# Optimization experiments

Measured on AMD Instinct MI355X. Metric: run time of the kernel, lower is better.

The kernel has to match this reference:

```python
import jax, jax.numpy as jnp
import numpy as np

N_ENT = 100000
NUM_REL = 400  # includes inverse relations
IN_DIM = 128
OUT_DIM = 128
NUM_EDGES = 800000  # first half 'in' direction, second half 'out' direction


def setup_inputs() -> dict:
    key = jax.random.key(0)
    ks = jax.random.split(key, 10)
    s = 1.0 / np.sqrt(IN_DIM)
    return {
        "x": jax.random.normal(ks[0], (N_ENT, IN_DIM), jnp.float32),
        "r": jax.random.normal(ks[1], (NUM_REL, IN_DIM), jnp.float32),
        "edge_index": jax.random.randint(ks[2], (2, NUM_EDGES), 0, N_ENT, jnp.int32),
        "edge_type": jax.random.randint(ks[3], (NUM_EDGES,), 0, NUM_REL, jnp.int32),
        "w_in": jax.random.normal(ks[4], (IN_DIM, OUT_DIM), jnp.float32) * s,
        "w_out": jax.random.normal(ks[5], (IN_DIM, OUT_DIM), jnp.float32) * s,
        "w_loop": jax.random.normal(ks[6], (IN_DIM, OUT_DIM), jnp.float32) * s,
        "w_rel": jax.random.normal(ks[7], (IN_DIM, OUT_DIM), jnp.float32) * s,
        "loop_rel": jax.random.normal(ks[8], (1, IN_DIM), jnp.float32) * s,
        "bias": jnp.zeros((OUT_DIM,), jnp.float32),
    }


def _edge_norm(row, col, n_ent, dtype):
    # symmetric normalization deg^-1/2[row] * deg^-1/2[col], deg from row (dst) degrees
    deg = jnp.zeros((n_ent,), dtype).at[row].add(1.0)
    dinv = jnp.where(deg > 0, 1.0 / jnp.sqrt(jnp.maximum(deg, 1.0)), 0.0)
    return dinv[row] * dinv[col]


def _propagate(x, r_full, row, col, etype, w, norm):
    # gather-compose-transform-scatter: composition = sub (h_j - h_r)
    h_j = x[col]                     # [E, D]
    h_r = r_full[etype]              # [E, D]
    msg = (h_j - h_r) @ w            # [E, out_dim]
    if norm is not None:
        msg = msg * norm[:, None]
    return jnp.zeros((x.shape[0], w.shape[1]), x.dtype).at[row].add(msg)


def reference(x, r, edge_index, edge_type, w_in, w_out, w_loop, w_rel, loop_rel, bias):
    n_ent = x.shape[0]
    r_full = jnp.concatenate([r, loop_rel], axis=0)   # [R+1, D], last row = loop relation
    e_half = edge_index.shape[1] // 2
    row, col = edge_index[0], edge_index[1]

    # 'in' mode (first half of edges)
    ri, ci, ti = row[:e_half], col[:e_half], edge_type[:e_half]
    out_in = _propagate(x, r_full, ri, ci, ti, w_in, _edge_norm(ri, ci, n_ent, x.dtype))
    # 'out' mode (second half of edges)
    ro, co, to = row[e_half:], col[e_half:], edge_type[e_half:]
    out_out = _propagate(x, r_full, ro, co, to, w_out, _edge_norm(ro, co, n_ent, x.dtype))
    # 'loop' mode: self edges with loop relation, no edge norm
    loop_idx = jnp.arange(n_ent, dtype=edge_index.dtype)
    loop_type = jnp.full((n_ent,), r.shape[0], dtype=edge_type.dtype)
    out_loop = _propagate(x, r_full, loop_idx, loop_idx, loop_type, w_loop, None)

    out = (out_in + out_out + out_loop) * (1.0 / 3.0) + bias
    out = jnp.tanh(out)
    r_out = r_full[:-1] @ w_rel      # linear relation transformation (drop loop rel)
    return out, r_out
```

## Files before the change

### kernel.cpp

```cpp
#include <hip/hip_runtime.h>
#include <hip/hip_bf16.h>

#define N_ENT    100000
#define NUM_REL  400
#define DIM      128
#define NUM_EDGES 800000
#define E_HALF   400000
#define N_RB     6250
#define CAP      24

using short8 = __attribute__((ext_vector_type(8))) short;
using f32x4  = __attribute__((ext_vector_type(4))) float;

__device__ __forceinline__ float bf_lo(unsigned u) { return __uint_as_float(u << 16); }
__device__ __forceinline__ float bf_hi(unsigned u) { return __uint_as_float(u & 0xffff0000u); }
__device__ __forceinline__ unsigned short f2bf(float f) {
    unsigned u = __float_as_uint(f);
    u = u + 0x7fffu + ((u >> 16) & 1u);
    return (unsigned short)(u >> 16);
}
__device__ __forceinline__ unsigned pack2bf(float a, float b) {
    return (unsigned)f2bf(a) | ((unsigned)f2bf(b) << 16);
}

#define FB_FILL 3125
#define FB_XB   (FB_FILL + 6250)
#define FB_WT   (FB_XB + 24)
#define FB_RB   (FB_WT + 25)
#define FB_CV   (FB_RB + 1)
#define FB_REL  (FB_CV + 200)
__global__ __launch_bounds__(256) void mega_kernel(const int* __restrict__ rows,
                                                   const int* __restrict__ cols,
                                                   const int* __restrict__ et,
                                                   const float* __restrict__ x,
                                                   const float* __restrict__ w_in,
                                                   const float* __restrict__ w_out,
                                                   const float* __restrict__ w_loop,
                                                   const float* __restrict__ r,
                                                   const float* __restrict__ loop_rel,
                                                   const float* __restrict__ w_rel,
                                                   int* __restrict__ cursor,
                                                   unsigned* __restrict__ recs,
                                                   uint4* __restrict__ xb4,
                                                   uint4* __restrict__ wtfrag,
                                                   uint4* __restrict__ rb16,
                                                   float* __restrict__ cvec,
                                                   float* __restrict__ r_out) {
    int b = blockIdx.x;
    int t = threadIdx.x;
    if (b < FB_FILL) {
        int e = b * 256 + t;
        if (e < NUM_EDGES) {
            int half = (e >= E_HALF) ? 1 : 0;
            int g = half * N_ENT + rows[e];
            int col = cols[e];
            int ty = et[e];
            int pos = atomicAdd(&cursor[g], 1);
            if (pos < CAP)
                recs[(size_t)g * CAP + pos] = (unsigned)col | ((unsigned)ty << 17);
        }
    } else if (b < FB_XB) {
        int i = (b - FB_FILL) * 256 + t;
        const float* p = x + (size_t)(i >> 4) * DIM + (i & 15) * 8;
        float4 f0 = *(const float4*)p;
        float4 f1 = *(const float4*)(p + 4);
        uint4 o;
        o.x = pack2bf(f0.x, f0.y);
        o.y = pack2bf(f0.z, f0.w);
        o.z = pack2bf(f1.x, f1.y);
        o.w = pack2bf(f1.z, f1.w);
        xb4[i] = o;
    } else if (b < FB_WT) {
        int j = (b - FB_XB) * 256 + t;
        if (j < 8 * 12 * 64) {
            int lane = j & 63;
            int kb = (j >> 6) % 12;
            int nblk = j / 768;
            int n = nblk * 16 + (lane & 15);
            int s = kb >> 2;
            int klo = (kb & 3) * 32 + (lane >> 4) * 8;
            const float* W = (s == 0) ? w_in : (s == 1) ? w_out : w_loop;
            float v[8];
            #pragma unroll
            for (int e = 0; e < 8; ++e) v[e] = W[(klo + e) * DIM + n];
            uint4 o;
            o.x = pack2bf(v[0], v[1]);
            o.y = pack2bf(v[2], v[3]);
            o.z = pack2bf(v[4], v[5]);
            o.w = pack2bf(v[6], v[7]);
            wtfrag[j] = o;
        }
    } else if (b < FB_RB) {
        int k = (b - FB_WT) * 256 + t;
        if (k < NUM_REL * 16) {
            const float* p = r + (size_t)(k >> 4) * DIM + (k & 15) * 8;
            float4 f0 = *(const float4*)p;
            float4 f1 = *(const float4*)(p + 4);
            uint4 o;
            o.x = pack2bf(f0.x, f0.y);
            o.y = pack2bf(f0.z, f0.w);
            o.z = pack2bf(f1.x, f1.y);
            o.w = pack2bf(f1.z, f1.w);
            rb16[k] = o;
        }
    } else if (b < FB_CV) {
        if (t < 128) {
            float acc = 0.0f;
            #pragma unroll 8
            for (int k = 0; k < DIM; ++k)
                acc += loop_rel[k] * w_loop[k * DIM + t];
            cvec[t] = acc;
        }
    } else {
        int row = (b - FB_CV) * 2 + (t >> 7);
        int col = t & 127;
        const float* rr = r + (size_t)row * DIM;
        float acc = 0.0f;
        #pragma unroll 8
        for (int k = 0; k < DIM; ++k)
            acc += rr[k] * w_rel[k * DIM + col];
        r_out[(size_t)row * DIM + col] = acc;
    }
}

#define ACC8(X, V, NRM)                                        \
    acc[0] += (NRM) * (bf_lo((X).x) - bf_lo((V).x));           \
    acc[1] += (NRM) * (bf_hi((X).x) - bf_hi((V).x));           \
    acc[2] += (NRM) * (bf_lo((X).y) - bf_lo((V).y));           \
    acc[3] += (NRM) * (bf_hi((X).y) - bf_hi((V).y));           \
    acc[4] += (NRM) * (bf_lo((X).z) - bf_lo((V).z));           \
    acc[5] += (NRM) * (bf_hi((X).z) - bf_hi((V).z));           \
    acc[6] += (NRM) * (bf_lo((X).w) - bf_lo((V).w));           \
    acc[7] += (NRM) * (bf_hi((X).w) - bf_hi((V).w));

__global__ __launch_bounds__(256) void gather_agg_kernel(const int* __restrict__ cursor,
                                                         const unsigned* __restrict__ recs,
                                                         const unsigned short* __restrict__ xb,
                                                         const unsigned short* __restrict__ rb16,
                                                         uint4* __restrict__ aggfrag) {
    int gid = blockIdx.x * 256 + threadIdx.x;
    int g = gid >> 4;
    if (g >= 2 * N_ENT) return;
    int c = gid & 15;
    int dg = cursor[g];
    int hb = (g >= N_ENT) ? N_ENT : 0;
    float acc[8] = {0.f, 0.f, 0.f, 0.f, 0.f, 0.f, 0.f, 0.f};
    if (dg > 0) {
        int dgc = dg < CAP ? dg : CAP;
        float dgi = rsqrtf((float)dg);
        const unsigned* rb = recs + (size_t)g * CAP;
        int e = 0;
        for (; e + 4 <= dgc; e += 4) {
            unsigned r0 = rb[e], r1 = rb[e + 1], r2 = rb[e + 2], r3 = rb[e + 3];
            int c0 = r0 & 0x1ffff, t0 = r0 >> 17;
            int c1 = r1 & 0x1ffff, t1 = r1 >> 17;
            int c2 = r2 & 0x1ffff, t2 = r2 >> 17;
            int c3 = r3 & 0x1ffff, t3 = r3 >> 17;
            int d0 = cursor[hb + c0];
            int d1 = cursor[hb + c1];
            int d2 = cursor[hb + c2];
            int d3 = cursor[hb + c3];
            uint4 x0 = ((const uint4*)(xb + (size_t)c0 * DIM))[c];
            uint4 v0 = ((const uint4*)(rb16 + (size_t)t0 * DIM))[c];
            uint4 x1 = ((const uint4*)(xb + (size_t)c1 * DIM))[c];
            uint4 v1 = ((const uint4*)(rb16 + (size_t)t1 * DIM))[c];
            uint4 x2 = ((const uint4*)(xb + (size_t)c2 * DIM))[c];
            uint4 v2 = ((const uint4*)(rb16 + (size_t)t2 * DIM))[c];
            uint4 x3 = ((const uint4*)(xb + (size_t)c3 * DIM))[c];
            uint4 v3 = ((const uint4*)(rb16 + (size_t)t3 * DIM))[c];
            float n0 = (d0 > 0) ? dgi * rsqrtf((float)d0) : 0.0f;
            float n1 = (d1 > 0) ? dgi * rsqrtf((float)d1) : 0.0f;
            float n2 = (d2 > 0) ? dgi * rsqrtf((float)d2) : 0.0f;
            float n3 = (d3 > 0) ? dgi * rsqrtf((float)d3) : 0.0f;
            ACC8(x0, v0, n0)
            ACC8(x1, v1, n1)
            ACC8(x2, v2, n2)
            ACC8(x3, v3, n3)
        }
        for (; e < dgc; ++e) {
            unsigned rA = rb[e];
            int cA = rA & 0x1ffff, tA = rA >> 17;
            int dA = cursor[hb + cA];
            uint4 xA = ((const uint4*)(xb + (size_t)cA * DIM))[c];
            uint4 vA = ((const uint4*)(rb16 + (size_t)tA * DIM))[c];
            float nA = (dA > 0) ? dgi * rsqrtf((float)dA) : 0.0f;
            ACC8(xA, vA, nA)
        }
    }
    uint4 o;
    o.x = pack2bf(acc[0], acc[1]);
    o.y = pack2bf(acc[2], acc[3]);
    o.z = pack2bf(acc[4], acc[5]);
    o.w = pack2bf(acc[6], acc[7]);
    aggfrag[(((g >> 4) * 4 + (c >> 2)) * 64) + (c & 3) * 16 + (g & 15)] = o;
}

__global__ __launch_bounds__(256) void mfma_gemm_kernel(const uint4* __restrict__ aggfrag,
                                                        const unsigned short* __restrict__ xb,
                                                        const uint4* __restrict__ wtfrag,
                                                        const float* __restrict__ bias,
                                                        const float* __restrict__ cvec,
                                                        float* __restrict__ out) {
    __shared__ float plds[2][32][65];

    int tid = threadIdx.x;
    int wave = tid >> 6;
    int lane = tid & 63;
    int wn = wave & 1;
    int kh = wave >> 1;
    int lr = lane & 15;
    int ks = lane >> 4;
    int rbb = blockIdx.x * 2;
    int row0 = blockIdx.x * 32;

    uint4 ua[2][6];
    #pragma unroll
    for (int j = 0; j < 6; ++j) {
        int kb = kh * 6 + j;
        int s = kb >> 2, kq = kb & 3;
        #pragma unroll
        for (int mi = 0; mi < 2; ++mi) {
            if (s < 2) {
                ua[mi][j] = aggfrag[((size_t)(rbb + mi + s * N_RB) * 4 + kq) * 64 + lane];
            } else {
                int row = (rbb + mi) * 16 + lr;
                ua[mi][j] = *(const uint4*)(xb + (size_t)row * DIM + kq * 32 + ks * 8);
            }
        }
    }

    f32x4 acc[2][4];
    #pragma unroll
    for (int mi = 0; mi < 2; ++mi)
        #pragma unroll
        for (int ni = 0; ni < 4; ++ni)
            acc[mi][ni] = (f32x4){0.f, 0.f, 0.f, 0.f};

    #pragma unroll
    for (int j = 0; j < 6; ++j) {
        int kb = kh * 6 + j;
        short8 b[4];
        #pragma unroll
        for (int ni = 0; ni < 4; ++ni) {
            uint4 u = wtfrag[((wn * 4 + ni) * 12 + kb) * 64 + lane];
            b[ni] = *(short8*)&u;
        }
        #pragma unroll
        for (int mi = 0; mi < 2; ++mi) {
            short8 a = *(short8*)&ua[mi][j];
            #pragma unroll
            for (int ni = 0; ni < 4; ++ni)
                acc[mi][ni] = __builtin_amdgcn_mfma_f32_16x16x32_bf16(a, b[ni], acc[mi][ni], 0, 0, 0);
        }
    }

    if (kh == 1) {
        #pragma unroll
        for (int mi = 0; mi < 2; ++mi)
            #pragma unroll
            for (int ni = 0; ni < 4; ++ni)
                #pragma unroll
                for (int reg = 0; reg < 4; ++reg)
                    plds[wn][mi * 16 + ks * 4 + reg][ni * 16 + lr] = acc[mi][ni][reg];
    }
    __syncthreads();
    if (kh == 1) return;

    int col0 = wn * 64;
    const float third = 1.0f / 3.0f;
    float bb[4];
    #pragma unroll
    for (int ni = 0; ni < 4; ++ni) {
        int col = col0 + ni * 16 + lr;
        bb[ni] = bias[col] - third * cvec[col];
    }

    #pragma unroll
    for (int mi = 0; mi < 2; ++mi) {
        #pragma unroll
        for (int reg = 0; reg < 4; ++reg) {
            int rl = mi * 16 + ks * 4 + reg;
            int grow = row0 + rl;
            #pragma unroll
            for (int ni = 0; ni < 4; ++ni) {
                float v = acc[mi][ni][reg] + plds[wn][rl][ni * 16 + lr];
                out[(size_t)grow * DIM + col0 + ni * 16 + lr] = tanhf(v * third + bb[ni]);
            }
        }
    }
}

extern "C" void kernel_launch(void* const* d_in, const int* in_sizes, int n_in,
                              void* d_out, int out_size, void* d_ws, size_t ws_size,
                              hipStream_t stream) {
    const float* x        = (const float*)d_in[0];
    const float* r        = (const float*)d_in[1];
    const int*   ei       = (const int*)d_in[2];
    const int*   et       = (const int*)d_in[3];
    const float* w_in     = (const float*)d_in[4];
    const float* w_out    = (const float*)d_in[5];
    const float* w_loop   = (const float*)d_in[6];
    const float* w_rel    = (const float*)d_in[7];
    const float* loop_rel = (const float*)d_in[8];
    const float* bias     = (const float*)d_in[9];

    float* out   = (float*)d_out;
    float* r_out = out + (size_t)N_ENT * DIM;

    unsigned short* aggf = (unsigned short*)d_ws;
    unsigned short* xb   = aggf + 2ull * N_ENT * DIM;
    unsigned short* wtf  = xb + (size_t)N_ENT * DIM;
    unsigned short* rb16 = wtf + 8 * 12 * 64 * 8;
    unsigned* recs = (unsigned*)(rb16 + NUM_REL * DIM);
    int*   cursor  = (int*)(recs + 2ull * N_ENT * CAP);
    float* cvec    = (float*)(cursor + 2 * N_ENT);

    const int* rows = ei;
    const int* cols = ei + NUM_EDGES;

    hipMemsetAsync(cursor, 0, 2ull * N_ENT * sizeof(int), stream);

    mega_kernel<<<FB_REL, 256, 0, stream>>>(
        rows, cols, et, x, w_in, w_out, w_loop, r, loop_rel, w_rel,
        cursor, recs, (uint4*)xb, (uint4*)wtf, (uint4*)rb16, cvec, r_out);

    gather_agg_kernel<<<(2 * N_ENT * 16 + 255) / 256, 256, 0, stream>>>(
        cursor, recs, xb, rb16, (uint4*)aggf);

    mfma_gemm_kernel<<<N_ENT / 32, 256, 0, stream>>>(
        (const uint4*)aggf, xb, (const uint4*)wtf, bias, cvec, out);
}
```

Baseline: 151.4 us.

## Split gather edges across four lane groups per node and coarsen fill blocks

The gather kernel now gives each node a full wave: four 16-lane groups each take one edge of every group of four and combine partial sums with cross-lane shuffles. Records are read as one vector load per iteration. The aim is more memory parallelism per node and less serial looping for high-degree nodes. The fill stage also has each thread handle four strided edges, which cuts the number of fill blocks. The cost is shuffle reductions and idle lanes for low-degree nodes, since average degree is about four.

```diff
diff --git a/kernel.cpp b/kernel.cpp
--- a/kernel.cpp
+++ b/kernel.cpp
@@ -23,7 +23,8 @@
     return (unsigned)f2bf(a) | ((unsigned)f2bf(b) << 16);
 }
 
-#define FB_FILL 3125
+#define FILL_T  200192
+#define FB_FILL 782
 #define FB_XB   (FB_FILL + 6250)
 #define FB_WT   (FB_XB + 24)
 #define FB_RB   (FB_WT + 25)
@@ -49,15 +50,19 @@
     int b = blockIdx.x;
     int t = threadIdx.x;
     if (b < FB_FILL) {
-        int e = b * 256 + t;
-        if (e < NUM_EDGES) {
-            int half = (e >= E_HALF) ? 1 : 0;
-            int g = half * N_ENT + rows[e];
-            int col = cols[e];
-            int ty = et[e];
-            int pos = atomicAdd(&cursor[g], 1);
-            if (pos < CAP)
-                recs[(size_t)g * CAP + pos] = (unsigned)col | ((unsigned)ty << 17);
+        int base = b * 256 + t;
+        #pragma unroll
+        for (int k = 0; k < 4; ++k) {
+            int e = base + k * FILL_T;
+            if (e < NUM_EDGES) {
+                int half = (e >= E_HALF) ? 1 : 0;
+                int g = half * N_ENT + rows[e];
+                int col = cols[e];
+                int ty = et[e];
+                int pos = atomicAdd(&cursor[g], 1);
+                if (pos < CAP)
+                    recs[(size_t)g * CAP + pos] = (unsigned)col | ((unsigned)ty << 17);
+            }
         }
     } else if (b < FB_XB) {
         int i = (b - FB_FILL) * 256 + t;
@@ -138,10 +143,10 @@
                                                          const unsigned short* __restrict__ xb,
                                                          const unsigned short* __restrict__ rb16,
                                                          uint4* __restrict__ aggfrag) {
-    int gid = blockIdx.x * 256 + threadIdx.x;
-    int g = gid >> 4;
-    if (g >= 2 * N_ENT) return;
-    int c = gid & 15;
+    int lane = threadIdx.x & 63;
+    int g = blockIdx.x * 4 + (threadIdx.x >> 6);
+    int q = lane >> 4;
+    int c = lane & 15;
     int dg = cursor[g];
     int hb = (g >= N_ENT) ? N_ENT : 0;
     float acc[8] = {0.f, 0.f, 0.f, 0.f, 0.f, 0.f, 0.f, 0.f};
@@ -149,50 +154,35 @@
         int dgc = dg < CAP ? dg : CAP;
         float dgi = rsqrtf((float)dg);
         const unsigned* rb = recs + (size_t)g * CAP;
-        int e = 0;
-        for (; e + 4 <= dgc; e += 4) {
-            unsigned r0 = rb[e], r1 = rb[e + 1], r2 = rb[e + 2], r3 = rb[e + 3];
-            int c0 = r0 & 0x1ffff, t0 = r0 >> 17;
-            int c1 = r1 & 0x1ffff, t1 = r1 >> 17;
-            int c2 = r2 & 0x1ffff, t2 = r2 >> 17;
-            int c3 = r3 & 0x1ffff, t3 = r3 >> 17;
-            int d0 = cursor[hb + c0];
-            int d1 = cursor[hb + c1];
-            int d2 = cursor[hb + c2];
-            int d3 = cursor[hb + c3];
-            uint4 x0 = ((const uint4*)(xb + (size_t)c0 * DIM))[c];
-            uint4 v0 = ((const uint4*)(rb16 + (size_t)t0 * DIM))[c];
-            uint4 x1 = ((const uint4*)(xb + (size_t)c1 * DIM))[c];
-            uint4 v1 = ((const uint4*)(rb16 + (size_t)t1 * DIM))[c];
-            uint4 x2 = ((const uint4*)(xb + (size_t)c2 * DIM))[c];
-            uint4 v2 = ((const uint4*)(rb16 + (size_t)t2 * DIM))[c];
-            uint4 x3 = ((const uint4*)(xb + (size_t)c3 * DIM))[c];
-            uint4 v3 = ((const uint4*)(rb16 + (size_t)t3 * DIM))[c];
-            float n0 = (d0 > 0) ? dgi * rsqrtf((float)d0) : 0.0f;
-            float n1 = (d1 > 0) ? dgi * rsqrtf((float)d1) : 0.0f;
-            float n2 = (d2 > 0) ? dgi * rsqrtf((float)d2) : 0.0f;
-            float n3 = (d3 > 0) ? dgi * rsqrtf((float)d3) : 0.0f;
-            ACC8(x0, v0, n0)
-            ACC8(x1, v1, n1)
-            ACC8(x2, v2, n2)
-            ACC8(x3, v3, n3)
-        }
-        for (; e < dgc; ++e) {
-            unsigned rA = rb[e];
-            int cA = rA & 0x1ffff, tA = rA >> 17;
-            int dA = cursor[hb + cA];
-            uint4 xA = ((const uint4*)(xb + (size_t)cA * DIM))[c];
-            uint4 vA = ((const uint4*)(rb16 + (size_t)tA * DIM))[c];
-            float nA = (dA > 0) ? dgi * rsqrtf((float)dA) : 0.0f;
-            ACC8(xA, vA, nA)
-        }
-    }
-    uint4 o;
-    o.x = pack2bf(acc[0], acc[1]);
-    o.y = pack2bf(acc[2], acc[3]);
-    o.z = pack2bf(acc[4], acc[5]);
-    o.w = pack2bf(acc[6], acc[7]);
-    aggfrag[(((g >> 4) * 4 + (c >> 2)) * 64) + (c & 3) * 16 + (g & 15)] = o;
+        int iters = (dgc + 3) >> 2;
+        for (int i = 0; i < iters; ++i) {
+            uint4 u = *(const uint4*)(rb + i * 4);
+            int idx = i * 4 + q;
+            unsigned rec = (q & 2) ? ((q & 1) ? u.w : u.z) : ((q & 1) ? u.y : u.x);
+            bool valid = idx < dgc;
+            rec = valid ? rec : 0u;
+            int col = rec & 0x1ffff;
+            int ty = rec >> 17;
+            int d = cursor[hb + col];
+            float n = (valid && d > 0) ? dgi * rsqrtf((float)d) : 0.0f;
+            uint4 xv = ((const uint4*)(xb + (size_t)col * DIM))[c];
+            uint4 rv = ((const uint4*)(rb16 + (size_t)ty * DIM))[c];
+            ACC8(xv, rv, n)
+        }
+    }
+    #pragma unroll
+    for (int k = 0; k < 8; ++k) {
+        acc[k] += __shfl_xor(acc[k], 16);
+        acc[k] += __shfl_xor(acc[k], 32);
+    }
+    if (q == 0) {
+        uint4 o;
+        o.x = pack2bf(acc[0], acc[1]);
+        o.y = pack2bf(acc[2], acc[3]);
+        o.z = pack2bf(acc[4], acc[5]);
+        o.w = pack2bf(acc[6], acc[7]);
+        aggfrag[(((g >> 4) * 4 + (c >> 2)) * 64) + (c & 3) * 16 + (g & 15)] = o;
+    }
 }
 
 __global__ __launch_bounds__(256) void mfma_gemm_kernel(const uint4* __restrict__ aggfrag,
@@ -324,7 +314,7 @@
         rows, cols, et, x, w_in, w_out, w_loop, r, loop_rel, w_rel,
         cursor, recs, (uint4*)xb, (uint4*)wtf, (uint4*)rb16, cvec, r_out);
 
-    gather_agg_kernel<<<(2 * N_ENT * 16 + 255) / 256, 256, 0, stream>>>(
+    gather_agg_kernel<<<2 * N_ENT / 4, 256, 0, stream>>>(
         cursor, recs, xb, rb16, (uint4*)aggf);
 
     mfma_gemm_kernel<<<N_ENT / 32, 256, 0, stream>>>(
```

Measured after the change: 167.1 us. 10.4% more time.
